# Optimization experiments

Measured on AMD Instinct MI355X. Metric: run time of the kernel, lower is better.

Reference implementation:

```python
import jax, jax.numpy as jnp
import numpy as np
import math

N_HEAD = 16
HEAD_DIM = 64
N_EMBD = N_HEAD * HEAD_DIM  # 1024


def _alibi_slopes(n_heads):
    def pow2(n):
        start = 2.0 ** (-2.0 ** (-(math.log2(n) - 3)))
        return [start * (start ** i) for i in range(n)]
    if n_heads & (n_heads - 1) == 0:
        s = pow2(n_heads)
    else:
        cp2 = 2 ** math.floor(math.log2(n_heads))
        s = pow2(cp2)
        extra_base = 2.0 ** (-2.0 ** (-(math.log2(2 * cp2) - 3)))
        s += [extra_base * (extra_base ** i) for i in range(n_heads - cp2)]
        s = s[:n_heads]
    return jnp.asarray(np.array(s, dtype=np.float32))


def setup_inputs() -> dict:
    key = jax.random.key(0)
    k1, k2, k3, k4 = jax.random.split(key, 4)
    B, T = 2, 2048
    x = jax.random.normal(k1, (B, T, N_EMBD), dtype=jnp.float32)
    # c_attn weight for q,k (use_v=True -> 2*n_embd outputs), no bias
    W_attn = jax.random.normal(k2, (N_EMBD, 2 * N_EMBD), dtype=jnp.float32) * 0.02
    v_tmp = jax.random.normal(k3, (N_HEAD, N_HEAD), dtype=jnp.float32) * 0.02
    proj_tmp = jax.random.normal(k4, (N_HEAD, N_HEAD), dtype=jnp.float32) * 0.02
    return {"x": x, "W_attn": W_attn, "v_tmp": v_tmp, "proj_tmp": proj_tmp}


def reference(x, W_attn, v_tmp, proj_tmp):
    B, T, C = x.shape
    H, D = N_HEAD, HEAD_DIM
    scale = 1.0 / math.sqrt(D)

    qk = x @ W_attn  # (B,T,2C)
    q, k = qk[..., :C], qk[..., C:]
    q = q.reshape(B, T, H, D).transpose(0, 2, 1, 3)  # (B,H,T,D)
    k = k.reshape(B, T, H, D).transpose(0, 2, 1, 3)

    # V via Kronecker-lifted matrix: x @ kron(v_tmp, I_D)
    # block structure => mix head channels: out[...,j,d] = sum_i x[...,i,d]*v_tmp[i,j]
    xh = x.reshape(B, T, H, D)
    v = jnp.einsum('btid,ij->btjd', xh, v_tmp)  # (B,T,H,D)

    scores = jnp.einsum('bhqd,bhkd->bhqk', q, k) * scale  # (B,H,T,T)

    # ALiBi bias + causal mask
    pos = jnp.arange(T, dtype=jnp.float32)
    rel = pos[None, :] - pos[:, None]  # (T,T), mem - ctx
    slopes = _alibi_slopes(H)
    bias = slopes[:, None, None] * rel[None, :, :]
    causal = pos[None, :] <= pos[:, None]
    bias = jnp.where(causal[None, :, :], bias, -jnp.inf)
    scores = scores + bias[None]

    att = jax.nn.softmax(scores, axis=-1)
    y = jnp.einsum('bhqk,bkhd->bqhd', att, v)  # (B,T,H,D)

    # output proj via kron(proj_tmp, I_D).T: out[...,i,d] = sum_j y[...,j,d]*proj_tmp[i,j]
    y = jnp.einsum('btjd,ij->btid', y, proj_tmp)
    return y.reshape(B, T, C)
```

## Files before the change

kernel.cpp:

```cpp
#include <hip/hip_runtime.h>

typedef __attribute__((ext_vector_type(8))) __bf16 bf16x8;
typedef __attribute__((ext_vector_type(8))) unsigned short u16x8;
typedef __attribute__((ext_vector_type(4))) float f32x4;

#define LOG2E 1.4426950408889634f

#define GLDS16(gp, lp)                                                \
  __builtin_amdgcn_global_load_lds(                                   \
      (const __attribute__((address_space(1))) void*)(gp),            \
      (__attribute__((address_space(3))) void*)(lp), 16, 0, 0)

__device__ __forceinline__ unsigned short f2b(float f) {
  return __builtin_bit_cast(unsigned short, (__bf16)f);
}
__device__ __forceinline__ float b2f(unsigned short h) {
  return __uint_as_float(((unsigned)h) << 16);
}

__global__ __launch_bounds__(256) void k_xv(const float* __restrict__ x,
                                            const float* __restrict__ vt,
                                            unsigned short* __restrict__ xb,
                                            unsigned short* __restrict__ vb) {
  __shared__ float s_vt[256];
  s_vt[threadIdx.x] = vt[threadIdx.x];
  __syncthreads();
  int g = blockIdx.x * 256 + threadIdx.x;
  int bt = g >> 6, d = g & 63;
  const float* xp = x + (size_t)bt * 1024 + d;
  float xi[16];
#pragma unroll
  for (int i = 0; i < 16; ++i) xi[i] = xp[i * 64];
#pragma unroll
  for (int i = 0; i < 16; ++i) xb[(size_t)bt * 1024 + i * 64 + d] = f2b(xi[i]);
#pragma unroll
  for (int j = 0; j < 16; ++j) {
    float s = 0.f;
#pragma unroll
    for (int i = 0; i < 16; ++i) s += xi[i] * s_vt[i * 16 + j];
    vb[(size_t)bt * 1024 + j * 64 + d] = f2b(s);
  }
}

__global__ __launch_bounds__(256) void k_trans_w(const float* __restrict__ W,
                                                 unsigned short* __restrict__ Wt) {
  __shared__ unsigned short tile[64][65];
  int n0 = blockIdx.x * 64;
  int k0 = blockIdx.y * 64;
  int tx = threadIdx.x & 63, ty = threadIdx.x >> 6;
#pragma unroll
  for (int r = 0; r < 16; ++r) {
    int kk = ty * 16 + r;
    tile[kk][tx] = f2b(W[(size_t)(k0 + kk) * 2048 + n0 + tx]);
  }
  __syncthreads();
#pragma unroll
  for (int r = 0; r < 16; ++r) {
    int nn = ty * 16 + r;
    Wt[(size_t)(n0 + nn) * 1024 + k0 + tx] = tile[tx][nn];
  }
}

__global__ __launch_bounds__(256) void k_gemm_qk(const unsigned short* __restrict__ A,
                                                 const unsigned short* __restrict__ Bt,
                                                 unsigned short* __restrict__ C) {
  __shared__ unsigned short As[128 * 32];
  __shared__ unsigned short Bs[128 * 32];
  const int K = 1024;
  int m0 = blockIdx.x * 128;
  int n0 = blockIdx.y * 128;
  int tid = threadIdx.x;
  int w = tid >> 6, lane = tid & 63;
  int lq = lane & 15, lk8 = (lane >> 4) * 8;
  int wr = (w >> 1) * 64, wc = (w & 1) * 64;
  f32x4 acc[4][4];
#pragma unroll
  for (int i = 0; i < 4; ++i)
#pragma unroll
    for (int j = 0; j < 4; ++j)
#pragma unroll
      for (int r = 0; r < 4; ++r) acc[i][j][r] = 0.f;

  for (int kk = 0; kk < K; kk += 32) {
    __syncthreads();
#pragma unroll
    for (int i = 0; i < 2; ++i) {
      int c = tid + 256 * i;
      int row = c >> 2, col = (c & 3) * 8;
      GLDS16(A + (size_t)(m0 + row) * K + kk + col, As + c * 8);
      GLDS16(Bt + (size_t)(n0 + row) * K + kk + col, Bs + c * 8);
    }
    __syncthreads();
    bf16x8 af[4], bf[4];
#pragma unroll
    for (int i = 0; i < 4; ++i) af[i] = *(const bf16x8*)(As + (wr + i * 16 + lq) * 32 + lk8);
#pragma unroll
    for (int j = 0; j < 4; ++j) bf[j] = *(const bf16x8*)(Bs + (wc + j * 16 + lq) * 32 + lk8);
#pragma unroll
    for (int i = 0; i < 4; ++i)
#pragma unroll
      for (int j = 0; j < 4; ++j)
        acc[i][j] = __builtin_amdgcn_mfma_f32_16x16x32_bf16(af[i], bf[j], acc[i][j], 0, 0, 0);
  }
#pragma unroll
  for (int i = 0; i < 4; ++i)
#pragma unroll
    for (int j = 0; j < 4; ++j)
#pragma unroll
      for (int r = 0; r < 4; ++r) {
        int m = m0 + wr + i * 16 + (lane >> 4) * 4 + r;
        int n = n0 + wc + j * 16 + lq;
        C[(size_t)m * 2048 + n] = f2b(acc[i][j][r]);
      }
}

__global__ __launch_bounds__(256) void k_vtrans(const unsigned short* __restrict__ vb,
                                                unsigned short* __restrict__ Vt) {
  __shared__ unsigned short tile[64][65];
  int t0 = blockIdx.x * 64;
  int c0 = blockIdx.y * 64;
  int b = blockIdx.z;
  int tx = threadIdx.x & 63, ty = threadIdx.x >> 6;
#pragma unroll
  for (int r = 0; r < 16; ++r) {
    int tt = ty * 16 + r;
    tile[tt][tx] = vb[((size_t)b * 2048 + t0 + tt) * 1024 + c0 + tx];
  }
  __syncthreads();
#pragma unroll
  for (int r = 0; r < 16; ++r) {
    int cc = ty * 16 + r;
    Vt[((size_t)b * 1024 + c0 + cc) * 2048 + t0 + tx] = tile[tx][cc];
  }
}

__global__ __launch_bounds__(256) void k_flash(const unsigned short* __restrict__ qkb,
                                               const unsigned short* __restrict__ Vt,
                                               unsigned short* __restrict__ y) {
  __shared__ unsigned short Ks[2][2][64 * 32];
  __shared__ unsigned short Vs[2][2][64 * 32];
  __shared__ unsigned short Pbuf[4][16 * 64];
  int id = blockIdx.x;
  int xcd = id & 7, s = id >> 3;
  int grp = xcd + 8 * (s & 3);
  int qt = 31 - (s >> 2);
  int hd = grp & 15, b = grp >> 4;
  int tid = threadIdx.x;
  int w = tid >> 6, lane = tid & 63;
  int quad = lane >> 4, lq = lane & 15, lk8 = quad * 8;
  int rs = tid >> 2, cs = (tid & 3) * 8;
  const size_t rowb = (size_t)b * 2048;
  const size_t vrow = ((size_t)b * 1024 + hd * 64 + rs) * 2048 + cs;
  const size_t krow = ((rowb + rs) << 11) + 1024 + hd * 64 + cs;

  float slope = exp2f(-0.5f * (float)(hd + 1));
  const float c1 = 0.125f * LOG2E;
  const float c2 = slope * LOG2E;
  const float SHIFT = 16.0f;

  bf16x8 ones;
#pragma unroll
  for (int i = 0; i < 8; ++i) ones[i] = (__bf16)1.0f;

  int q0 = qt * 64;
  int qg = q0 + w * 16 + lq;
  bf16x8 qf0 = *(const bf16x8*)(qkb + ((rowb + qg) << 11) + hd * 64 + lk8);
  bf16x8 qf1 = *(const bf16x8*)(qkb + ((rowb + qg) << 11) + hd * 64 + 32 + lk8);
  int qrow_base = q0 + w * 16 + quad * 4;

  float base_b[4][4];
#pragma unroll
  for (int s4 = 0; s4 < 4; ++s4)
#pragma unroll
    for (int r = 0; r < 4; ++r)
      base_b[s4][r] = c2 * (float)(s4 * 16 + lq - qrow_base - r) - SHIFT;

  f32x4 o[4], o4;
#pragma unroll
  for (int r = 0; r < 4; ++r) o4[r] = 0.f;
#pragma unroll
  for (int jj = 0; jj < 4; ++jj)
#pragma unroll
    for (int r = 0; r < 4; ++r) o[jj][r] = 0.f;

  GLDS16(qkb + krow,      &Ks[0][0][rs * 32 + cs]);
  GLDS16(qkb + krow + 32, &Ks[0][1][rs * 32 + cs]);
  GLDS16(Vt + vrow,       &Vs[0][0][rs * 32 + cs]);
  GLDS16(Vt + vrow + 32,  &Vs[0][1][rs * 32 + cs]);
  __syncthreads();
  int cur = 0;

#pragma unroll 1
  for (int kt = 0; kt <= qt; ++kt) {
    int k0 = kt * 64;
    if (kt < qt) {
      size_t koff = (size_t)(k0 + 64);
      int nxt = cur ^ 1;
      GLDS16(qkb + krow + (koff << 11),      &Ks[nxt][0][rs * 32 + cs]);
      GLDS16(qkb + krow + (koff << 11) + 32, &Ks[nxt][1][rs * 32 + cs]);
      GLDS16(Vt + vrow + koff,               &Vs[nxt][0][rs * 32 + cs]);
      GLDS16(Vt + vrow + koff + 32,          &Vs[nxt][1][rs * 32 + cs]);
    }
    bf16x8 kc[4][2];
#pragma unroll
    for (int s4 = 0; s4 < 4; ++s4) {
      u16x8 t0 = *(const u16x8*)(&Ks[cur][0][(s4 * 16 + lq) * 32 + lk8]);
      u16x8 t1 = *(const u16x8*)(&Ks[cur][1][(s4 * 16 + lq) * 32 + lk8]);
      kc[s4][0] = __builtin_bit_cast(bf16x8, t0);
      kc[s4][1] = __builtin_bit_cast(bf16x8, t1);
    }
    f32x4 S[4];
#pragma unroll
    for (int s4 = 0; s4 < 4; ++s4) {
      f32x4 a;
#pragma unroll
      for (int r = 0; r < 4; ++r) a[r] = 0.f;
      a = __builtin_amdgcn_mfma_f32_16x16x32_bf16(qf0, kc[s4][0], a, 0, 0, 0);
      a = __builtin_amdgcn_mfma_f32_16x16x32_bf16(qf1, kc[s4][1], a, 0, 0, 0);
      S[s4] = a;
    }
    float bk = c2 * (float)k0;
    float p[4][4];
    if (kt == qt) {
#pragma unroll
      for (int s4 = 0; s4 < 4; ++s4) {
        int kg = k0 + s4 * 16 + lq;
#pragma unroll
        for (int r = 0; r < 4; ++r) {
          int qr = qrow_base + r;
          float v = S[s4][r] * c1 + (base_b[s4][r] + bk);
          v = (kg <= qr) ? v : -1e30f;
          p[s4][r] = exp2f(v);
        }
      }
    } else {
#pragma unroll
      for (int s4 = 0; s4 < 4; ++s4) {
#pragma unroll
        for (int r = 0; r < 4; ++r) {
          float v = S[s4][r] * c1 + (base_b[s4][r] + bk);
          p[s4][r] = exp2f(v);
        }
      }
    }
#pragma unroll
    for (int s4 = 0; s4 < 4; ++s4) {
      int cg = (s4 ^ quad) << 4;
#pragma unroll
      for (int r = 0; r < 4; ++r)
        Pbuf[w][(quad * 4 + r) * 64 + cg + lq] = f2b(p[s4][r]);
    }
    int g0 = ((quad >> 1) ^ (lq >> 2)) << 4;
    int g1 = ((2 | (quad >> 1)) ^ (lq >> 2)) << 4;
    int sub = (quad & 1) * 8;
    u16x8 t0 = *(const u16x8*)(&Pbuf[w][lq * 64 + g0 + sub]);
    u16x8 t1 = *(const u16x8*)(&Pbuf[w][lq * 64 + g1 + sub]);
    bf16x8 pf0 = __builtin_bit_cast(bf16x8, t0);
    bf16x8 pf1 = __builtin_bit_cast(bf16x8, t1);
#pragma unroll
    for (int jj = 0; jj < 4; ++jj) {
      u16x8 v0 = *(const u16x8*)(&Vs[cur][0][(jj * 16 + lq) * 32 + lk8]);
      u16x8 v1 = *(const u16x8*)(&Vs[cur][1][(jj * 16 + lq) * 32 + lk8]);
      bf16x8 vf0 = __builtin_bit_cast(bf16x8, v0);
      bf16x8 vf1 = __builtin_bit_cast(bf16x8, v1);
      o[jj] = __builtin_amdgcn_mfma_f32_16x16x32_bf16(pf0, vf0, o[jj], 0, 0, 0);
      o[jj] = __builtin_amdgcn_mfma_f32_16x16x32_bf16(pf1, vf1, o[jj], 0, 0, 0);
      if (jj == 0) {
        o4 = __builtin_amdgcn_mfma_f32_16x16x32_bf16(pf0, ones, o4, 0, 0, 0);
        o4 = __builtin_amdgcn_mfma_f32_16x16x32_bf16(pf1, ones, o4, 0, 0, 0);
      }
    }
    if (kt < qt) {
      __syncthreads();
      cur ^= 1;
    }
  }
#pragma unroll
  for (int r = 0; r < 4; ++r) {
    float inv = 1.0f / o4[r];
    int qr = qrow_base + r;
#pragma unroll
    for (int jj = 0; jj < 4; ++jj)
      y[((rowb + qr) << 10) + hd * 64 + jj * 16 + lq] = f2b(o[jj][r] * inv);
  }
}

__global__ __launch_bounds__(256) void k_proj(const unsigned short* __restrict__ yb,
                                              const float* __restrict__ pt,
                                              float* __restrict__ out) {
  __shared__ float s_pt[256];
  s_pt[threadIdx.x] = pt[threadIdx.x];
  __syncthreads();
  int g = blockIdx.x * 256 + threadIdx.x;
  int bt = g >> 6, d = g & 63;
  float yj[16];
#pragma unroll
  for (int j = 0; j < 16; ++j) yj[j] = b2f(yb[(size_t)bt * 1024 + j * 64 + d]);
#pragma unroll
  for (int i = 0; i < 16; ++i) {
    float s = 0.f;
#pragma unroll
    for (int j = 0; j < 16; ++j) s += yj[j] * s_pt[i * 16 + j];
    out[(size_t)bt * 1024 + i * 64 + d] = s;
  }
}

extern "C" void kernel_launch(void* const* d_in, const int* in_sizes, int n_in,
                              void* d_out, int out_size, void* d_ws, size_t ws_size,
                              hipStream_t stream) {
  const float* x  = (const float*)d_in[0];
  const float* W  = (const float*)d_in[1];
  const float* vt = (const float*)d_in[2];
  const float* pt = (const float*)d_in[3];
  float* out = (float*)d_out;

  char* ws = (char*)d_ws;
  unsigned short* xb  = (unsigned short*)(ws);
  unsigned short* Wt  = (unsigned short*)(ws + (8u  << 20));
  unsigned short* qkb = (unsigned short*)(ws + (12u << 20));
  unsigned short* vb  = (unsigned short*)(ws + (28u << 20));
  unsigned short* Vtr = (unsigned short*)(ws + (36u << 20));
  unsigned short* yb  = xb;

  k_xv     <<<1024, 256, 0, stream>>>(x, vt, xb, vb);
  k_trans_w<<<dim3(32, 16), 256, 0, stream>>>(W, Wt);
  k_gemm_qk<<<dim3(32, 16), 256, 0, stream>>>(xb, Wt, qkb);
  k_vtrans <<<dim3(32, 16, 2), 256, 0, stream>>>(vb, Vtr);
  k_flash  <<<1024, 256, 0, stream>>>(qkb, Vtr, yb);
  k_proj   <<<1024, 256, 0, stream>>>(yb, pt, out);
}
```

Before: 164.8 us.

## Merge prep kernels, transpose flash MFMA to keep P in registers, swizzle LDS

Merges the x/V conversion with the W transpose, and the QK GEMM with the V transpose, into two launches that branch on block index, cutting the launch count from six to four. In the flash kernel the MFMA operands are swapped so scores come out transposed. P is then packed to bf16 with cvt_pk and rearranged with permlane swaps instead of a round trip through an LDS buffer. K/V LDS tiles get an XOR swizzle to reduce bank conflicts, launch bounds ask for 4 blocks per CU, and output stores become vectorized. The risks are correctness of the permlane layout and register pressure from the occupancy hint.

```diff
diff --git a/kernel.cpp b/kernel.cpp
--- a/kernel.cpp
+++ b/kernel.cpp
@@ -3,6 +3,7 @@
 typedef __attribute__((ext_vector_type(8))) __bf16 bf16x8;
 typedef __attribute__((ext_vector_type(8))) unsigned short u16x8;
 typedef __attribute__((ext_vector_type(4))) float f32x4;
+typedef __attribute__((ext_vector_type(4))) unsigned int u32x4;
 
 #define LOG2E 1.4426950408889634f
 
@@ -17,129 +18,143 @@
 __device__ __forceinline__ float b2f(unsigned short h) {
   return __uint_as_float(((unsigned)h) << 16);
 }
-
-__global__ __launch_bounds__(256) void k_xv(const float* __restrict__ x,
-                                            const float* __restrict__ vt,
-                                            unsigned short* __restrict__ xb,
-                                            unsigned short* __restrict__ vb) {
-  __shared__ float s_vt[256];
-  s_vt[threadIdx.x] = vt[threadIdx.x];
-  __syncthreads();
-  int g = blockIdx.x * 256 + threadIdx.x;
-  int bt = g >> 6, d = g & 63;
-  const float* xp = x + (size_t)bt * 1024 + d;
-  float xi[16];
-#pragma unroll
-  for (int i = 0; i < 16; ++i) xi[i] = xp[i * 64];
-#pragma unroll
-  for (int i = 0; i < 16; ++i) xb[(size_t)bt * 1024 + i * 64 + d] = f2b(xi[i]);
-#pragma unroll
-  for (int j = 0; j < 16; ++j) {
-    float s = 0.f;
-#pragma unroll
-    for (int i = 0; i < 16; ++i) s += xi[i] * s_vt[i * 16 + j];
-    vb[(size_t)bt * 1024 + j * 64 + d] = f2b(s);
-  }
-}
-
-__global__ __launch_bounds__(256) void k_trans_w(const float* __restrict__ W,
-                                                 unsigned short* __restrict__ Wt) {
-  __shared__ unsigned short tile[64][65];
-  int n0 = blockIdx.x * 64;
-  int k0 = blockIdx.y * 64;
-  int tx = threadIdx.x & 63, ty = threadIdx.x >> 6;
-#pragma unroll
-  for (int r = 0; r < 16; ++r) {
-    int kk = ty * 16 + r;
-    tile[kk][tx] = f2b(W[(size_t)(k0 + kk) * 2048 + n0 + tx]);
-  }
-  __syncthreads();
-#pragma unroll
-  for (int r = 0; r < 16; ++r) {
-    int nn = ty * 16 + r;
-    Wt[(size_t)(n0 + nn) * 1024 + k0 + tx] = tile[tx][nn];
-  }
-}
-
-__global__ __launch_bounds__(256) void k_gemm_qk(const unsigned short* __restrict__ A,
-                                                 const unsigned short* __restrict__ Bt,
-                                                 unsigned short* __restrict__ C) {
-  __shared__ unsigned short As[128 * 32];
-  __shared__ unsigned short Bs[128 * 32];
-  const int K = 1024;
-  int m0 = blockIdx.x * 128;
-  int n0 = blockIdx.y * 128;
-  int tid = threadIdx.x;
-  int w = tid >> 6, lane = tid & 63;
-  int lq = lane & 15, lk8 = (lane >> 4) * 8;
-  int wr = (w >> 1) * 64, wc = (w & 1) * 64;
-  f32x4 acc[4][4];
-#pragma unroll
-  for (int i = 0; i < 4; ++i)
-#pragma unroll
-    for (int j = 0; j < 4; ++j)
-#pragma unroll
-      for (int r = 0; r < 4; ++r) acc[i][j][r] = 0.f;
-
-  for (int kk = 0; kk < K; kk += 32) {
+__device__ __forceinline__ unsigned cvt_pk(float a, float b) {
+  unsigned r;
+  asm("v_cvt_pk_bf16_f32 %0, %1, %2" : "=v"(r) : "v"(a), "v"(b));
+  return r;
+}
+__device__ __forceinline__ void swap32(unsigned& a, unsigned& b) {
+  asm("v_permlane32_swap_b32 %0, %1" : "+v"(a), "+v"(b));
+}
+__device__ __forceinline__ void swap16(unsigned& a, unsigned& b) {
+  asm("v_permlane16_swap_b32 %0, %1" : "+v"(a), "+v"(b));
+}
+
+__global__ __launch_bounds__(256) void k_pre(const float* __restrict__ x,
+                                             const float* __restrict__ vt,
+                                             const float* __restrict__ W,
+                                             unsigned short* __restrict__ xb,
+                                             unsigned short* __restrict__ vb,
+                                             unsigned short* __restrict__ Wt) {
+  if (blockIdx.x < 1024) {
+    __shared__ float s_vt[256];
+    s_vt[threadIdx.x] = vt[threadIdx.x];
     __syncthreads();
-#pragma unroll
-    for (int i = 0; i < 2; ++i) {
-      int c = tid + 256 * i;
-      int row = c >> 2, col = (c & 3) * 8;
-      GLDS16(A + (size_t)(m0 + row) * K + kk + col, As + c * 8);
-      GLDS16(Bt + (size_t)(n0 + row) * K + kk + col, Bs + c * 8);
+    int g = blockIdx.x * 256 + threadIdx.x;
+    int bt = g >> 6, d = g & 63;
+    const float* xp = x + (size_t)bt * 1024 + d;
+    float xi[16];
+#pragma unroll
+    for (int i = 0; i < 16; ++i) xi[i] = xp[i * 64];
+#pragma unroll
+    for (int i = 0; i < 16; ++i) xb[(size_t)bt * 1024 + i * 64 + d] = f2b(xi[i]);
+#pragma unroll
+    for (int j = 0; j < 16; ++j) {
+      float s = 0.f;
+#pragma unroll
+      for (int i = 0; i < 16; ++i) s += xi[i] * s_vt[i * 16 + j];
+      vb[(size_t)bt * 1024 + j * 64 + d] = f2b(s);
+    }
+  } else {
+    __shared__ unsigned short tile[64][65];
+    int id2 = blockIdx.x - 1024;
+    int n0 = (id2 & 31) * 64;
+    int k0 = (id2 >> 5) * 64;
+    int tx = threadIdx.x & 63, ty = threadIdx.x >> 6;
+#pragma unroll
+    for (int r = 0; r < 16; ++r) {
+      int kk = ty * 16 + r;
+      tile[kk][tx] = f2b(W[(size_t)(k0 + kk) * 2048 + n0 + tx]);
     }
     __syncthreads();
-    bf16x8 af[4], bf[4];
-#pragma unroll
-    for (int i = 0; i < 4; ++i) af[i] = *(const bf16x8*)(As + (wr + i * 16 + lq) * 32 + lk8);
-#pragma unroll
-    for (int j = 0; j < 4; ++j) bf[j] = *(const bf16x8*)(Bs + (wc + j * 16 + lq) * 32 + lk8);
+#pragma unroll
+    for (int r = 0; r < 16; ++r) {
+      int nn = ty * 16 + r;
+      Wt[(size_t)(n0 + nn) * 1024 + k0 + tx] = tile[tx][nn];
+    }
+  }
+}
+
+__global__ __launch_bounds__(256) void k_mid(const unsigned short* __restrict__ A,
+                                             const unsigned short* __restrict__ Bt,
+                                             unsigned short* __restrict__ C,
+                                             const unsigned short* __restrict__ vb,
+                                             unsigned short* __restrict__ Vt) {
+  if (blockIdx.x < 512) {
+    __shared__ unsigned short As[128 * 32];
+    __shared__ unsigned short Bs[128 * 32];
+    const int K = 1024;
+    int m0 = (blockIdx.x & 31) * 128;
+    int n0 = (blockIdx.x >> 5) * 128;
+    int tid = threadIdx.x;
+    int w = tid >> 6, lane = tid & 63;
+    int lq = lane & 15, lk8 = (lane >> 4) * 8;
+    int wr = (w >> 1) * 64, wc = (w & 1) * 64;
+    f32x4 acc[4][4];
 #pragma unroll
     for (int i = 0; i < 4; ++i)
 #pragma unroll
       for (int j = 0; j < 4; ++j)
-        acc[i][j] = __builtin_amdgcn_mfma_f32_16x16x32_bf16(af[i], bf[j], acc[i][j], 0, 0, 0);
-  }
-#pragma unroll
-  for (int i = 0; i < 4; ++i)
-#pragma unroll
-    for (int j = 0; j < 4; ++j)
-#pragma unroll
-      for (int r = 0; r < 4; ++r) {
-        int m = m0 + wr + i * 16 + (lane >> 4) * 4 + r;
-        int n = n0 + wc + j * 16 + lq;
-        C[(size_t)m * 2048 + n] = f2b(acc[i][j][r]);
+#pragma unroll
+        for (int r = 0; r < 4; ++r) acc[i][j][r] = 0.f;
+
+    for (int kk = 0; kk < K; kk += 32) {
+      __syncthreads();
+#pragma unroll
+      for (int i = 0; i < 2; ++i) {
+        int c = tid + 256 * i;
+        int row = c >> 2, col = (c & 3) * 8;
+        GLDS16(A + (size_t)(m0 + row) * K + kk + col, As + c * 8);
+        GLDS16(Bt + (size_t)(n0 + row) * K + kk + col, Bs + c * 8);
       }
-}
-
-__global__ __launch_bounds__(256) void k_vtrans(const unsigned short* __restrict__ vb,
-                                                unsigned short* __restrict__ Vt) {
-  __shared__ unsigned short tile[64][65];
-  int t0 = blockIdx.x * 64;
-  int c0 = blockIdx.y * 64;
-  int b = blockIdx.z;
-  int tx = threadIdx.x & 63, ty = threadIdx.x >> 6;
-#pragma unroll
-  for (int r = 0; r < 16; ++r) {
-    int tt = ty * 16 + r;
-    tile[tt][tx] = vb[((size_t)b * 2048 + t0 + tt) * 1024 + c0 + tx];
-  }
-  __syncthreads();
-#pragma unroll
-  for (int r = 0; r < 16; ++r) {
-    int cc = ty * 16 + r;
-    Vt[((size_t)b * 1024 + c0 + cc) * 2048 + t0 + tx] = tile[tx][cc];
-  }
-}
-
-__global__ __launch_bounds__(256) void k_flash(const unsigned short* __restrict__ qkb,
-                                               const unsigned short* __restrict__ Vt,
-                                               unsigned short* __restrict__ y) {
+      __syncthreads();
+      bf16x8 af[4], bf[4];
+#pragma unroll
+      for (int i = 0; i < 4; ++i) af[i] = *(const bf16x8*)(As + (wr + i * 16 + lq) * 32 + lk8);
+#pragma unroll
+      for (int j = 0; j < 4; ++j) bf[j] = *(const bf16x8*)(Bs + (wc + j * 16 + lq) * 32 + lk8);
+#pragma unroll
+      for (int i = 0; i < 4; ++i)
+#pragma unroll
+        for (int j = 0; j < 4; ++j)
+          acc[i][j] = __builtin_amdgcn_mfma_f32_16x16x32_bf16(af[i], bf[j], acc[i][j], 0, 0, 0);
+    }
+#pragma unroll
+    for (int i = 0; i < 4; ++i)
+#pragma unroll
+      for (int j = 0; j < 4; ++j)
+#pragma unroll
+        for (int r = 0; r < 4; ++r) {
+          int m = m0 + wr + i * 16 + (lane >> 4) * 4 + r;
+          int n = n0 + wc + j * 16 + lq;
+          C[(size_t)m * 2048 + n] = f2b(acc[i][j][r]);
+        }
+  } else {
+    __shared__ unsigned short tile[64][65];
+    int id2 = blockIdx.x - 512;
+    int t0 = (id2 & 31) * 64;
+    int c0 = ((id2 >> 5) & 15) * 64;
+    int b = id2 >> 9;
+    int tx = threadIdx.x & 63, ty = threadIdx.x >> 6;
+#pragma unroll
+    for (int r = 0; r < 16; ++r) {
+      int tt = ty * 16 + r;
+      tile[tt][tx] = vb[((size_t)b * 2048 + t0 + tt) * 1024 + c0 + tx];
+    }
+    __syncthreads();
+#pragma unroll
+    for (int r = 0; r < 16; ++r) {
+      int cc = ty * 16 + r;
+      Vt[((size_t)b * 1024 + c0 + cc) * 2048 + t0 + tx] = tile[tx][cc];
+    }
+  }
+}
+
+__global__ __launch_bounds__(256, 4) void k_flash(const unsigned short* __restrict__ qkb,
+                                                  const unsigned short* __restrict__ Vt,
+                                                  unsigned short* __restrict__ y) {
   __shared__ unsigned short Ks[2][2][64 * 32];
   __shared__ unsigned short Vs[2][2][64 * 32];
-  __shared__ unsigned short Pbuf[4][16 * 64];
   int id = blockIdx.x;
   int xcd = id & 7, s = id >> 3;
   int grp = xcd + 8 * (s & 3);
@@ -148,10 +163,12 @@
   int tid = threadIdx.x;
   int w = tid >> 6, lane = tid & 63;
   int quad = lane >> 4, lq = lane & 15, lk8 = quad * 8;
-  int rs = tid >> 2, cs = (tid & 3) * 8;
+  int xk8 = (quad ^ ((lq >> 1) & 3)) * 8;
+  int rs = tid >> 2;
+  int csw = ((tid & 3) ^ ((tid >> 3) & 3)) * 8;
   const size_t rowb = (size_t)b * 2048;
-  const size_t vrow = ((size_t)b * 1024 + hd * 64 + rs) * 2048 + cs;
-  const size_t krow = ((rowb + rs) << 11) + 1024 + hd * 64 + cs;
+  const size_t vrow = ((size_t)b * 1024 + hd * 64 + rs) * 2048 + csw;
+  const size_t krow = ((rowb + rs) << 11) + 1024 + hd * 64 + csw;
 
   float slope = exp2f(-0.5f * (float)(hd + 1));
   const float c1 = 0.125f * LOG2E;
@@ -163,17 +180,16 @@
   for (int i = 0; i < 8; ++i) ones[i] = (__bf16)1.0f;
 
   int q0 = qt * 64;
-  int qg = q0 + w * 16 + lq;
-  bf16x8 qf0 = *(const bf16x8*)(qkb + ((rowb + qg) << 11) + hd * 64 + lk8);
-  bf16x8 qf1 = *(const bf16x8*)(qkb + ((rowb + qg) << 11) + hd * 64 + 32 + lk8);
-  int qrow_base = q0 + w * 16 + quad * 4;
+  int qr_l = q0 + w * 16 + lq;
+  bf16x8 qf0 = *(const bf16x8*)(qkb + ((rowb + qr_l) << 11) + hd * 64 + lk8);
+  bf16x8 qf1 = *(const bf16x8*)(qkb + ((rowb + qr_l) << 11) + hd * 64 + 32 + lk8);
 
   float base_b[4][4];
 #pragma unroll
   for (int s4 = 0; s4 < 4; ++s4)
 #pragma unroll
     for (int r = 0; r < 4; ++r)
-      base_b[s4][r] = c2 * (float)(s4 * 16 + lq - qrow_base - r) - SHIFT;
+      base_b[s4][r] = c2 * (float)(s4 * 16 + quad * 4 + r - qr_l) - SHIFT;
 
   f32x4 o[4], o4;
 #pragma unroll
@@ -183,10 +199,10 @@
 #pragma unroll
     for (int r = 0; r < 4; ++r) o[jj][r] = 0.f;
 
-  GLDS16(qkb + krow,      &Ks[0][0][rs * 32 + cs]);
-  GLDS16(qkb + krow + 32, &Ks[0][1][rs * 32 + cs]);
-  GLDS16(Vt + vrow,       &Vs[0][0][rs * 32 + cs]);
-  GLDS16(Vt + vrow + 32,  &Vs[0][1][rs * 32 + cs]);
+  GLDS16(qkb + krow,      &Ks[0][0][rs * 32 + (tid & 3) * 8]);
+  GLDS16(qkb + krow + 32, &Ks[0][1][rs * 32 + (tid & 3) * 8]);
+  GLDS16(Vt + vrow,       &Vs[0][0][rs * 32 + (tid & 3) * 8]);
+  GLDS16(Vt + vrow + 32,  &Vs[0][1][rs * 32 + (tid & 3) * 8]);
   __syncthreads();
   int cur = 0;
 
@@ -196,16 +212,16 @@
     if (kt < qt) {
       size_t koff = (size_t)(k0 + 64);
       int nxt = cur ^ 1;
-      GLDS16(qkb + krow + (koff << 11),      &Ks[nxt][0][rs * 32 + cs]);
-      GLDS16(qkb + krow + (koff << 11) + 32, &Ks[nxt][1][rs * 32 + cs]);
-      GLDS16(Vt + vrow + koff,               &Vs[nxt][0][rs * 32 + cs]);
-      GLDS16(Vt + vrow + koff + 32,          &Vs[nxt][1][rs * 32 + cs]);
+      GLDS16(qkb + krow + (koff << 11),      &Ks[nxt][0][rs * 32 + (tid & 3) * 8]);
+      GLDS16(qkb + krow + (koff << 11) + 32, &Ks[nxt][1][rs * 32 + (tid & 3) * 8]);
+      GLDS16(Vt + vrow + koff,               &Vs[nxt][0][rs * 32 + (tid & 3) * 8]);
+      GLDS16(Vt + vrow + koff + 32,          &Vs[nxt][1][rs * 32 + (tid & 3) * 8]);
     }
     bf16x8 kc[4][2];
 #pragma unroll
     for (int s4 = 0; s4 < 4; ++s4) {
-      u16x8 t0 = *(const u16x8*)(&Ks[cur][0][(s4 * 16 + lq) * 32 + lk8]);
-      u16x8 t1 = *(const u16x8*)(&Ks[cur][1][(s4 * 16 + lq) * 32 + lk8]);
+      u16x8 t0 = *(const u16x8*)(&Ks[cur][0][(s4 * 16 + lq) * 32 + xk8]);
+      u16x8 t1 = *(const u16x8*)(&Ks[cur][1][(s4 * 16 + lq) * 32 + xk8]);
       kc[s4][0] = __builtin_bit_cast(bf16x8, t0);
       kc[s4][1] = __builtin_bit_cast(bf16x8, t1);
     }
@@ -215,73 +231,72 @@
       f32x4 a;
 #pragma unroll
       for (int r = 0; r < 4; ++r) a[r] = 0.f;
-      a = __builtin_amdgcn_mfma_f32_16x16x32_bf16(qf0, kc[s4][0], a, 0, 0, 0);
-      a = __builtin_amdgcn_mfma_f32_16x16x32_bf16(qf1, kc[s4][1], a, 0, 0, 0);
+      a = __builtin_amdgcn_mfma_f32_16x16x32_bf16(kc[s4][0], qf0, a, 0, 0, 0);
+      a = __builtin_amdgcn_mfma_f32_16x16x32_bf16(kc[s4][1], qf1, a, 0, 0, 0);
       S[s4] = a;
     }
     float bk = c2 * (float)k0;
     float p[4][4];
     if (kt == qt) {
 #pragma unroll
-      for (int s4 = 0; s4 < 4; ++s4) {
-        int kg = k0 + s4 * 16 + lq;
+      for (int s4 = 0; s4 < 4; ++s4)
 #pragma unroll
         for (int r = 0; r < 4; ++r) {
-          int qr = qrow_base + r;
           float v = S[s4][r] * c1 + (base_b[s4][r] + bk);
-          v = (kg <= qr) ? v : -1e30f;
+          v = (k0 + s4 * 16 + quad * 4 + r <= qr_l) ? v : -1e30f;
           p[s4][r] = exp2f(v);
         }
-      }
     } else {
 #pragma unroll
-      for (int s4 = 0; s4 < 4; ++s4) {
+      for (int s4 = 0; s4 < 4; ++s4)
 #pragma unroll
         for (int r = 0; r < 4; ++r) {
           float v = S[s4][r] * c1 + (base_b[s4][r] + bk);
           p[s4][r] = exp2f(v);
         }
-      }
-    }
+    }
+    unsigned pk[4][2];
 #pragma unroll
     for (int s4 = 0; s4 < 4; ++s4) {
-      int cg = (s4 ^ quad) << 4;
-#pragma unroll
-      for (int r = 0; r < 4; ++r)
-        Pbuf[w][(quad * 4 + r) * 64 + cg + lq] = f2b(p[s4][r]);
-    }
-    int g0 = ((quad >> 1) ^ (lq >> 2)) << 4;
-    int g1 = ((2 | (quad >> 1)) ^ (lq >> 2)) << 4;
-    int sub = (quad & 1) * 8;
-    u16x8 t0 = *(const u16x8*)(&Pbuf[w][lq * 64 + g0 + sub]);
-    u16x8 t1 = *(const u16x8*)(&Pbuf[w][lq * 64 + g1 + sub]);
-    bf16x8 pf0 = __builtin_bit_cast(bf16x8, t0);
-    bf16x8 pf1 = __builtin_bit_cast(bf16x8, t1);
+      pk[s4][0] = cvt_pk(p[s4][0], p[s4][1]);
+      pk[s4][1] = cvt_pk(p[s4][2], p[s4][3]);
+    }
+    bf16x8 pf[2];
+#pragma unroll
+    for (int c = 0; c < 2; ++c) {
+      unsigned a0 = pk[2 * c][0], b0 = pk[2 * c + 1][0];
+      swap32(a0, b0); swap16(a0, b0);
+      unsigned a1 = pk[2 * c][1], b1 = pk[2 * c + 1][1];
+      swap32(a1, b1); swap16(a1, b1);
+      u32x4 t; t[0] = a0; t[1] = a1; t[2] = b0; t[3] = b1;
+      pf[c] = __builtin_bit_cast(bf16x8, t);
+    }
+    o4 = __builtin_amdgcn_mfma_f32_16x16x32_bf16(ones, pf[0], o4, 0, 0, 0);
+    o4 = __builtin_amdgcn_mfma_f32_16x16x32_bf16(ones, pf[1], o4, 0, 0, 0);
 #pragma unroll
     for (int jj = 0; jj < 4; ++jj) {
-      u16x8 v0 = *(const u16x8*)(&Vs[cur][0][(jj * 16 + lq) * 32 + lk8]);
-      u16x8 v1 = *(const u16x8*)(&Vs[cur][1][(jj * 16 + lq) * 32 + lk8]);
+      u16x8 v0 = *(const u16x8*)(&Vs[cur][0][(jj * 16 + lq) * 32 + xk8]);
+      u16x8 v1 = *(const u16x8*)(&Vs[cur][1][(jj * 16 + lq) * 32 + xk8]);
       bf16x8 vf0 = __builtin_bit_cast(bf16x8, v0);
       bf16x8 vf1 = __builtin_bit_cast(bf16x8, v1);
-      o[jj] = __builtin_amdgcn_mfma_f32_16x16x32_bf16(pf0, vf0, o[jj], 0, 0, 0);
-      o[jj] = __builtin_amdgcn_mfma_f32_16x16x32_bf16(pf1, vf1, o[jj], 0, 0, 0);
-      if (jj == 0) {
-        o4 = __builtin_amdgcn_mfma_f32_16x16x32_bf16(pf0, ones, o4, 0, 0, 0);
-        o4 = __builtin_amdgcn_mfma_f32_16x16x32_bf16(pf1, ones, o4, 0, 0, 0);
-      }
+      o[jj] = __builtin_amdgcn_mfma_f32_16x16x32_bf16(vf0, pf[0], o[jj], 0, 0, 0);
+      o[jj] = __builtin_amdgcn_mfma_f32_16x16x32_bf16(vf1, pf[1], o[jj], 0, 0, 0);
     }
     if (kt < qt) {
       __syncthreads();
       cur ^= 1;
     }
   }
-#pragma unroll
-  for (int r = 0; r < 4; ++r) {
-    float inv = 1.0f / o4[r];
-    int qr = qrow_base + r;
-#pragma unroll
-    for (int jj = 0; jj < 4; ++jj)
-      y[((rowb + qr) << 10) + hd * 64 + jj * 16 + lq] = f2b(o[jj][r] * inv);
+  float inv = 1.0f / o4[0];
+  size_t base = ((rowb + qr_l) << 10) + hd * 64 + quad * 4;
+#pragma unroll
+  for (int jj = 0; jj < 4; ++jj) {
+    ushort4 pk4;
+    pk4.x = f2b(o[jj][0] * inv);
+    pk4.y = f2b(o[jj][1] * inv);
+    pk4.z = f2b(o[jj][2] * inv);
+    pk4.w = f2b(o[jj][3] * inv);
+    *(ushort4*)(y + base + jj * 16) = pk4;
   }
 }
 
@@ -322,10 +337,8 @@
   unsigned short* Vtr = (unsigned short*)(ws + (36u << 20));
   unsigned short* yb  = xb;
 
-  k_xv     <<<1024, 256, 0, stream>>>(x, vt, xb, vb);
-  k_trans_w<<<dim3(32, 16), 256, 0, stream>>>(W, Wt);
-  k_gemm_qk<<<dim3(32, 16), 256, 0, stream>>>(xb, Wt, qkb);
-  k_vtrans <<<dim3(32, 16, 2), 256, 0, stream>>>(vb, Vtr);
-  k_flash  <<<1024, 256, 0, stream>>>(qkb, Vtr, yb);
-  k_proj   <<<1024, 256, 0, stream>>>(yb, pt, out);
-}
+  k_pre  <<<1536, 256, 0, stream>>>(x, vt, W, xb, vb, Wt);
+  k_mid  <<<1536, 256, 0, stream>>>(xb, Wt, qkb, vb, Vtr);
+  k_flash<<<1024, 256, 0, stream>>>(qkb, Vtr, yb);
+  k_proj <<<1024, 256, 0, stream>>>(yb, pt, out);
+}
```

New measurement: 153.3 us. 6.9% less time.
